# Optimization experiments

Hardware: AMD Instinct MI355X
Metric: run time of the kernel (lower is better)

Reference implementation:

```python
import jax, jax.numpy as jnp
import numpy as np

NUM_HEADS = 16


def setup_inputs() -> dict:
    key = jax.random.key(0)
    ks = jax.random.split(key, 5)
    B, N, D = 2, 2048, 1024
    scale = 1.0 / np.sqrt(D)  # roughly xavier-ish magnitude for weights
    return {
        "x": jax.random.normal(ks[0], (B, N, D), dtype=jnp.float32),
        "W_query": jax.random.normal(ks[1], (D, D), dtype=jnp.float32) * scale,
        "W_key": jax.random.normal(ks[2], (D, D), dtype=jnp.float32) * scale,
        "W_value": jax.random.normal(ks[3], (D, D), dtype=jnp.float32) * scale,
        "W_output": jax.random.normal(ks[4], (D, D), dtype=jnp.float32) * scale,
    }


def reference(x, W_query, W_key, W_value, W_output):
    # x: [B, N, D]; weights: [D, D]
    B, N, D = x.shape
    H = NUM_HEADS
    hd = D // H

    def mh_embed(W):
        # linear_embedding then split heads: [B, N, D] -> [B, H, N, hd]
        y = jnp.einsum("bnd,de->bne", x, W)
        return y.reshape(B, N, H, hd).transpose(0, 2, 1, 3)

    q = mh_embed(W_query)
    k = mh_embed(W_key)
    v = mh_embed(W_value)

    # NOTE: source scales by token_dim**-0.5 (full model dim), not head_dim
    attn = jnp.einsum("bhnd,bhmd->bhnm", q, k) * (D ** -0.5)
    attn = jax.nn.softmax(attn, axis=-1)
    out = jnp.einsum("bhnm,bhmd->bhnd", attn, v)  # [B, H, N, hd]

    out = out.transpose(0, 2, 1, 3).reshape(B, N, D)  # merge heads
    out = jnp.einsum("bnd,de->bne", out, W_output)
    return out
```

## Files before the change

### kernel.cpp

```cpp
#include <hip/hip_runtime.h>

#define D_MODEL 1024
#define N_TOK   2048
#define NHEAD   16
#define HDIM    64
#define BATCH   2
#define M_TOT   (BATCH*N_TOK)

typedef unsigned short u16;
typedef __bf16 bf16x8 __attribute__((ext_vector_type(8)));
typedef float  f32x4  __attribute__((ext_vector_type(4)));

#define QSCALE 0.04508422002777439f

__device__ __forceinline__ u16 f2bf(float f) {
  union { float f; unsigned u; } v; v.f = f;
  unsigned r = v.u + 0x7fffu + ((v.u >> 16) & 1u);
  return (u16)(r >> 16);
}

__device__ __forceinline__ unsigned pk2bf(float a, float b) {
#if __has_builtin(__builtin_amdgcn_cvt_pk_bf16_f32)
  typedef __bf16 bf16x2_t __attribute__((ext_vector_type(2)));
  bf16x2_t r = __builtin_amdgcn_cvt_pk_bf16_f32(a, b);
  union { bf16x2_t v; unsigned u; } c; c.v = r; return c.u;
#else
  return (unsigned)f2bf(a) | ((unsigned)f2bf(b) << 16);
#endif
}

__device__ __forceinline__ void gl2lds16(const void* g, void* l) {
  __builtin_amdgcn_global_load_lds(
      (__attribute__((address_space(1))) void*)g,
      (__attribute__((address_space(3))) void*)l, 16, 0, 0);
}

__global__ void prep_kernel(const float* __restrict__ x,
                            const float* __restrict__ s0, const float* __restrict__ s1,
                            const float* __restrict__ s2, const float* __restrict__ s3,
                            u16* __restrict__ xb,
                            u16* __restrict__ d0, u16* __restrict__ d1,
                            u16* __restrict__ d2, u16* __restrict__ d3) {
  const int t = threadIdx.y * 32 + threadIdx.x;
  if (blockIdx.z == 4) {
    int base = (blockIdx.y * 32 + blockIdx.x) * 256 + t;
#pragma unroll
    for (int r = 0; r < 4; ++r) {
      int i = base + r * 262144;
      float4 v = ((const float4*)x)[i];
      ushort4 o;
      o.x = f2bf(v.x); o.y = f2bf(v.y); o.z = f2bf(v.z); o.w = f2bf(v.w);
      ((ushort4*)xb)[i] = o;
    }
    return;
  }
  const float* src; u16* dst;
  switch (blockIdx.z) {
    case 0:  src = s0; dst = d0; break;
    case 1:  src = s1; dst = d1; break;
    case 2:  src = s2; dst = d2; break;
    default: src = s3; dst = d3; break;
  }
  float sc = (blockIdx.z == 0) ? QSCALE : 1.0f;
  __shared__ float tile[32][33];
  int xg = blockIdx.x * 32 + threadIdx.x;
  int ybase = blockIdx.y * 32;
#pragma unroll
  for (int r = 0; r < 4; ++r)
    tile[threadIdx.y + r*8][threadIdx.x] = src[(size_t)(ybase + threadIdx.y + r*8)*D_MODEL + xg];
  __syncthreads();
#pragma unroll
  for (int r = 0; r < 4; ++r)
    dst[(size_t)(blockIdx.x*32 + threadIdx.y + r*8)*D_MODEL + ybase + threadIdx.x] =
        f2bf(tile[threadIdx.x][threadIdx.y + r*8] * sc);
}

__device__ __forceinline__ void gemm_body(const u16* __restrict__ A,
                                          const u16* __restrict__ Bt,
                                          void* __restrict__ Cout, int mode) {
  __shared__ __attribute__((aligned(16))) u16 lA[128*32];
  __shared__ __attribute__((aligned(16))) u16 lB[128*32];
  const int t = threadIdx.x;
  const int lane = t & 63, w = t >> 6;
  const int wm = w >> 1, wn = w & 1;
  const int q4 = lane >> 4, l15 = lane & 15;
  const int m0 = blockIdx.y * 128, n0 = blockIdx.x * 128;

  f32x4 acc[4][4] = {};

  for (int k0 = 0; k0 < D_MODEL; k0 += 32) {
    __syncthreads();
#pragma unroll
    for (int i = 0; i < 2; ++i) {
      int c = i*256 + t;
      int row = c >> 2;
      int clog = (c & 3) ^ (row & 3);
      gl2lds16(A  + (size_t)(m0 + row)*D_MODEL + k0 + clog*8, lA + c*8);
      gl2lds16(Bt + (size_t)(n0 + row)*D_MODEL + k0 + clog*8, lB + c*8);
    }
    __syncthreads();
    bf16x8 af[4], bfr[4];
#pragma unroll
    for (int mi = 0; mi < 4; ++mi) {
      int r = wm*64 + mi*16 + l15;
      af[mi] = *(const bf16x8*)(lA + r*32 + ((q4 ^ (r & 3)) * 8));
    }
#pragma unroll
    for (int ni = 0; ni < 4; ++ni) {
      int r = wn*64 + ni*16 + l15;
      bfr[ni] = *(const bf16x8*)(lB + r*32 + ((q4 ^ (r & 3)) * 8));
    }
#pragma unroll
    for (int mi = 0; mi < 4; ++mi)
#pragma unroll
      for (int ni = 0; ni < 4; ++ni)
        acc[mi][ni] = __builtin_amdgcn_mfma_f32_16x16x32_bf16(af[mi], bfr[ni], acc[mi][ni], 0, 0, 0);
  }

#pragma unroll
  for (int mi = 0; mi < 4; ++mi) {
#pragma unroll
    for (int ni = 0; ni < 4; ++ni) {
      const int tok0 = m0 + wm*64 + mi*16 + q4*4;
      const int col  = n0 + wn*64 + ni*16 + l15;
      if (mode == 0) {
        u16* D = (u16*)Cout;
#pragma unroll
        for (int r = 0; r < 4; ++r) {
          int tok = tok0 + r;
          int b = tok >> 11, n = tok & (N_TOK-1);
          int h = col >> 6, d = col & (HDIM-1);
          D[(((size_t)(b*NHEAD + h))*N_TOK + n)*HDIM + d] = f2bf(acc[mi][ni][r]);
        }
      } else if (mode == 2) {
        int b = tok0 >> 11, n = tok0 & (N_TOK-1);
        int h = col >> 6, d = col & (HDIM-1);
        ushort4 pk;
        pk.x = f2bf(acc[mi][ni][0]); pk.y = f2bf(acc[mi][ni][1]);
        pk.z = f2bf(acc[mi][ni][2]); pk.w = f2bf(acc[mi][ni][3]);
        *(ushort4*)((u16*)Cout + ((size_t)(b*NHEAD + h)*HDIM + d)*N_TOK + n) = pk;
      } else {
        float* D = (float*)Cout;
#pragma unroll
        for (int r = 0; r < 4; ++r)
          D[(size_t)(tok0 + r)*D_MODEL + col] = acc[mi][ni][r];
      }
    }
  }
}

__global__ __launch_bounds__(256) void qkv_kernel(const u16* __restrict__ xb,
    const u16* __restrict__ wqt, const u16* __restrict__ wkt, const u16* __restrict__ wvt,
    u16* __restrict__ Q, u16* __restrict__ K, u16* __restrict__ Vt) {
  int z = blockIdx.z;
  const u16* B = (z == 0) ? wqt : (z == 1) ? wkt : wvt;
  void* C = (z == 0) ? (void*)Q : (z == 1) ? (void*)K : (void*)Vt;
  gemm_body(xb, B, C, (z == 2) ? 2 : 0);
}

__global__ __launch_bounds__(256) void out_kernel(const u16* __restrict__ ctx,
    const u16* __restrict__ wot, float* __restrict__ out) {
  gemm_body(ctx, wot, (void*)out, 3);
}

__global__ __launch_bounds__(256, 3) void attn_kernel(const u16* __restrict__ Qg,
    const u16* __restrict__ Kg, const u16* __restrict__ Vtg,
    float* __restrict__ Opart, float* __restrict__ Lpart) {
  __shared__ __attribute__((aligned(16))) u16 lds[24576];
  u16* lK = lds;
  u16* lV = lds + 8192;
  u16* lP = lds + 16384;
  const int t = threadIdx.x;
  const int lane = t & 63, w = t >> 6;
  const int q4 = lane >> 4, l15 = lane & 15;
  const int bh = blockIdx.y;
  const int qb = blockIdx.x >> 1, half = blockIdx.x & 1;
  const int qw0 = qb * 128 + w * 32;
  const size_t kvBase = (size_t)bh * (N_TOK * HDIM);
  u16* myP = lP + w * 2048;

  bf16x8 qf[2][2];
#pragma unroll
  for (int ni = 0; ni < 2; ++ni)
#pragma unroll
    for (int kk = 0; kk < 2; ++kk)
      qf[ni][kk] = *(const bf16x8*)(Qg + kvBase +
                    (size_t)(qw0 + ni*16 + l15)*HDIM + kk*32 + q4*8);

  f32x4 accO[4][2] = {};
  float lsum[2] = {0.f, 0.f};

  for (int it = 0; it < 8; ++it) {
    const int kv0 = half * 1024 + it * 128;
    __syncthreads();
#pragma unroll
    for (int i = 0; i < 4; ++i) {
      int c = i*256 + t;
      { int r = c >> 3, ch = c & 7;
        gl2lds16(Kg + kvBase + (size_t)(kv0 + r)*HDIM + ((ch ^ (r & 7)) * 8),
                 lK + c*8); }
      { int d = c >> 4, cv = c & 15;
        gl2lds16(Vtg + kvBase + (size_t)d*N_TOK + kv0 + ((cv ^ (d & 15)) * 8),
                 lV + c*8); }
    }
    __syncthreads();

#pragma unroll
    for (int h = 0; h < 2; ++h) {
#pragma unroll
      for (int mip = 0; mip < 4; ++mip) {
        const int mi = h*4 + mip;
        const int kv = mi*16 + l15;
        f32x4 s[2] = {};
#pragma unroll
        for (int kk = 0; kk < 2; ++kk) {
          bf16x8 a = *(const bf16x8*)(lK + kv*64 + (((kk*4 + q4) ^ (l15 & 7)) * 8));
#pragma unroll
          for (int ni = 0; ni < 2; ++ni)
            s[ni] = __builtin_amdgcn_mfma_f32_16x16x32_bf16(a, qf[ni][kk], s[ni], 0, 0, 0);
        }
#pragma unroll
        for (int ni = 0; ni < 2; ++ni) {
          float p0 = __builtin_amdgcn_exp2f(s[ni][0]);
          float p1 = __builtin_amdgcn_exp2f(s[ni][1]);
          float p2 = __builtin_amdgcn_exp2f(s[ni][2]);
          float p3 = __builtin_amdgcn_exp2f(s[ni][3]);
          lsum[ni] += (p0 + p1) + (p2 + p3);
          uint2 u; u.x = pk2bf(p0, p1); u.y = pk2bf(p2, p3);
          const int qloc = ni*16 + l15;
          const int kv8 = mip*4 + q4;
          *(uint2*)(myP + qloc*64 + (((kv8 >> 1) ^ (qloc & 7)) * 8) + (kv8 & 1)*4) = u;
        }
      }
#pragma unroll
      for (int kk2p = 0; kk2p < 2; ++kk2p) {
        bf16x8 bp[2];
#pragma unroll
        for (int ni = 0; ni < 2; ++ni)
          bp[ni] = *(const bf16x8*)(myP + (ni*16 + l15)*64 +
                                    (((kk2p*4 + q4) ^ (l15 & 7)) * 8));
#pragma unroll
        for (int mi2 = 0; mi2 < 4; ++mi2) {
          const int d = mi2*16 + l15;
          const int g = (h*2 + kk2p)*4 + q4;
          bf16x8 av = *(const bf16x8*)(lV + d*128 + ((g ^ (d & 15)) * 8));
#pragma unroll
          for (int ni = 0; ni < 2; ++ni)
            accO[mi2][ni] = __builtin_amdgcn_mfma_f32_16x16x32_bf16(av, bp[ni], accO[mi2][ni], 0, 0, 0);
        }
      }
    }
  }

  const int b = bh >> 4, head = bh & (NHEAD-1);
  float* Obase = Opart + (size_t)half * (M_TOT * D_MODEL);
#pragma unroll
  for (int ni = 0; ni < 2; ++ni) {
    float ls = lsum[ni];
    ls += __shfl_xor(ls, 16);
    ls += __shfl_xor(ls, 32);
    const int q = qw0 + ni*16 + l15;
    if (q4 == 0)
      Lpart[(size_t)half*(32*N_TOK) + bh*N_TOK + q] = ls;
    const size_t rb = ((size_t)(b*N_TOK + q))*D_MODEL + head*HDIM + q4*4;
#pragma unroll
    for (int mi2 = 0; mi2 < 4; ++mi2) {
      float4 v;
      v.x = accO[mi2][ni][0]; v.y = accO[mi2][ni][1];
      v.z = accO[mi2][ni][2]; v.w = accO[mi2][ni][3];
      *(float4*)(Obase + rb + mi2*16) = v;
    }
  }
}

__global__ __launch_bounds__(256) void combine_kernel(const float* __restrict__ Opart,
    const float* __restrict__ Lpart, u16* __restrict__ ctx) {
  int i = blockIdx.x * 256 + threadIdx.x;
  int tok = i >> 8, d4 = i & 255;
  int n = tok & (N_TOK-1), b = tok >> 11;
  int h = d4 >> 4;
  int bh = b*NHEAD + h;
  float l = Lpart[(size_t)bh*N_TOK + n] + Lpart[(size_t)(32*N_TOK) + bh*N_TOK + n];
  float inv = 1.0f / l;
  float4 o0 = *(const float4*)(Opart + (size_t)tok*D_MODEL + d4*4);
  float4 o1 = *(const float4*)(Opart + (size_t)(M_TOT*D_MODEL) + (size_t)tok*D_MODEL + d4*4);
  ushort4 o;
  o.x = f2bf((o0.x + o1.x) * inv);
  o.y = f2bf((o0.y + o1.y) * inv);
  o.z = f2bf((o0.z + o1.z) * inv);
  o.w = f2bf((o0.w + o1.w) * inv);
  *(ushort4*)(ctx + (size_t)tok*D_MODEL + d4*4) = o;
}

extern "C" void kernel_launch(void* const* d_in, const int* in_sizes, int n_in,
                              void* d_out, int out_size, void* d_ws, size_t ws_size,
                              hipStream_t stream) {
  const float* x  = (const float*)d_in[0];
  const float* Wq = (const float*)d_in[1];
  const float* Wk = (const float*)d_in[2];
  const float* Wv = (const float*)d_in[3];
  const float* Wo = (const float*)d_in[4];
  float* out = (float*)d_out;

  char* ws = (char*)d_ws;
  u16* xb   = (u16*)(ws);
  u16* wqt  = (u16*)(ws + (8u  << 20));
  u16* wkt  = (u16*)(ws + (10u << 20));
  u16* wvt  = (u16*)(ws + (12u << 20));
  u16* wot  = (u16*)(ws + (14u << 20));
  u16* Qw   = (u16*)(ws + (16u << 20));
  u16* Kw   = (u16*)(ws + (24u << 20));
  u16* Vtw  = (u16*)(ws + (32u << 20));
  u16* ctx  = (u16*)(ws + (40u << 20));
  float* Op = (float*)(ws + (48u << 20));
  float* Lp = (float*)(ws + (80u << 20));
  (void)in_sizes; (void)n_in; (void)out_size; (void)ws_size;

  prep_kernel<<<dim3(32, 32, 5), dim3(32, 8), 0, stream>>>(x, Wq, Wk, Wv, Wo,
                                                           xb, wqt, wkt, wvt, wot);
  qkv_kernel<<<dim3(8, 32, 3), 256, 0, stream>>>(xb, wqt, wkt, wvt, Qw, Kw, Vtw);
  attn_kernel<<<dim3(32, 32), 256, 0, stream>>>(Qw, Kw, Vtw, Op, Lp);
  combine_kernel<<<4096, 256, 0, stream>>>(Op, Lp, ctx);
  out_kernel<<<dim3(8, 32), 256, 0, stream>>>(ctx, wot, out);
}
```

Before: 203.1 us.

## Double-buffer LDS tiles in GEMM and attention to overlap loads with MFMA

Both the projection GEMM and the attention kernel now use two LDS buffers. The global-to-LDS loads for the next K step (GEMM) or KV tile (attention) are issued before the MFMA work on the current buffer, which removes one barrier per iteration and hides load latency. To keep total LDS the same, the attention KV tile shrinks from 128 to 64 tokens, with twice the iterations and a narrower V swizzle. The trade-off is more loop iterations and barriers in attention, plus doubled LDS in the GEMM, which may lower occupancy.

```diff
diff --git a/kernel.cpp b/kernel.cpp
--- a/kernel.cpp
+++ b/kernel.cpp
@@ -78,37 +78,47 @@
 __device__ __forceinline__ void gemm_body(const u16* __restrict__ A,
                                           const u16* __restrict__ Bt,
                                           void* __restrict__ Cout, int mode) {
-  __shared__ __attribute__((aligned(16))) u16 lA[128*32];
-  __shared__ __attribute__((aligned(16))) u16 lB[128*32];
+  __shared__ __attribute__((aligned(16))) u16 lA[2][128*32];
+  __shared__ __attribute__((aligned(16))) u16 lB[2][128*32];
   const int t = threadIdx.x;
   const int lane = t & 63, w = t >> 6;
   const int wm = w >> 1, wn = w & 1;
   const int q4 = lane >> 4, l15 = lane & 15;
   const int m0 = blockIdx.y * 128, n0 = blockIdx.x * 128;
 
+  const int c0 = t, c1 = 256 + t;
+  const int r0 = c0 >> 2, g0 = (c0 & 3) ^ (r0 & 3);
+  const int r1 = c1 >> 2, g1 = (c1 & 3) ^ (r1 & 3);
+
   f32x4 acc[4][4] = {};
 
-  for (int k0 = 0; k0 < D_MODEL; k0 += 32) {
+  gl2lds16(A  + (size_t)(m0 + r0)*D_MODEL + g0*8, &lA[0][c0*8]);
+  gl2lds16(Bt + (size_t)(n0 + r0)*D_MODEL + g0*8, &lB[0][c0*8]);
+  gl2lds16(A  + (size_t)(m0 + r1)*D_MODEL + g1*8, &lA[0][c1*8]);
+  gl2lds16(Bt + (size_t)(n0 + r1)*D_MODEL + g1*8, &lB[0][c1*8]);
+
+  for (int it = 0; it < 32; ++it) {
+    const int cur = it & 1;
     __syncthreads();
-#pragma unroll
-    for (int i = 0; i < 2; ++i) {
-      int c = i*256 + t;
-      int row = c >> 2;
-      int clog = (c & 3) ^ (row & 3);
-      gl2lds16(A  + (size_t)(m0 + row)*D_MODEL + k0 + clog*8, lA + c*8);
-      gl2lds16(Bt + (size_t)(n0 + row)*D_MODEL + k0 + clog*8, lB + c*8);
-    }
-    __syncthreads();
+    if (it + 1 < 32) {
+      const int kn = (it + 1) * 32;
+      u16* dA = &lA[cur ^ 1][0]; u16* dB = &lB[cur ^ 1][0];
+      gl2lds16(A  + (size_t)(m0 + r0)*D_MODEL + kn + g0*8, dA + c0*8);
+      gl2lds16(Bt + (size_t)(n0 + r0)*D_MODEL + kn + g0*8, dB + c0*8);
+      gl2lds16(A  + (size_t)(m0 + r1)*D_MODEL + kn + g1*8, dA + c1*8);
+      gl2lds16(Bt + (size_t)(n0 + r1)*D_MODEL + kn + g1*8, dB + c1*8);
+    }
+    const u16* sA = &lA[cur][0]; const u16* sB = &lB[cur][0];
     bf16x8 af[4], bfr[4];
 #pragma unroll
     for (int mi = 0; mi < 4; ++mi) {
       int r = wm*64 + mi*16 + l15;
-      af[mi] = *(const bf16x8*)(lA + r*32 + ((q4 ^ (r & 3)) * 8));
+      af[mi] = *(const bf16x8*)(sA + r*32 + ((q4 ^ (r & 3)) * 8));
     }
 #pragma unroll
     for (int ni = 0; ni < 4; ++ni) {
       int r = wn*64 + ni*16 + l15;
-      bfr[ni] = *(const bf16x8*)(lB + r*32 + ((q4 ^ (r & 3)) * 8));
+      bfr[ni] = *(const bf16x8*)(sB + r*32 + ((q4 ^ (r & 3)) * 8));
     }
 #pragma unroll
     for (int mi = 0; mi < 4; ++mi)
@@ -167,9 +177,6 @@
     const u16* __restrict__ Kg, const u16* __restrict__ Vtg,
     float* __restrict__ Opart, float* __restrict__ Lpart) {
   __shared__ __attribute__((aligned(16))) u16 lds[24576];
-  u16* lK = lds;
-  u16* lV = lds + 8192;
-  u16* lP = lds + 16384;
   const int t = threadIdx.x;
   const int lane = t & 63, w = t >> 6;
   const int q4 = lane >> 4, l15 = lane & 15;
@@ -177,7 +184,11 @@
   const int qb = blockIdx.x >> 1, half = blockIdx.x & 1;
   const int qw0 = qb * 128 + w * 32;
   const size_t kvBase = (size_t)bh * (N_TOK * HDIM);
-  u16* myP = lP + w * 2048;
+  u16* myP = lds + 16384 + w * 2048;
+
+  const int ck0 = t, ck1 = 256 + t;
+  const int kr0 = ck0 >> 3, kg0 = (ck0 & 7) ^ (kr0 & 7);
+  const int kr1 = ck1 >> 3, kg1 = (ck1 & 7) ^ (kr1 & 7);
 
   bf16x8 qf[2][2];
 #pragma unroll
@@ -190,64 +201,66 @@
   f32x4 accO[4][2] = {};
   float lsum[2] = {0.f, 0.f};
 
-  for (int it = 0; it < 8; ++it) {
-    const int kv0 = half * 1024 + it * 128;
+  const int kvStart = half * 1024;
+  gl2lds16(Kg  + kvBase + (size_t)(kvStart + kr0)*HDIM + kg0*8, lds + ck0*8);
+  gl2lds16(Kg  + kvBase + (size_t)(kvStart + kr1)*HDIM + kg1*8, lds + ck1*8);
+  gl2lds16(Vtg + kvBase + (size_t)kr0*N_TOK + kvStart + kg0*8,  lds + 8192 + ck0*8);
+  gl2lds16(Vtg + kvBase + (size_t)kr1*N_TOK + kvStart + kg1*8,  lds + 8192 + ck1*8);
+
+  for (int it = 0; it < 16; ++it) {
+    const int cur = it & 1;
     __syncthreads();
-#pragma unroll
-    for (int i = 0; i < 4; ++i) {
-      int c = i*256 + t;
-      { int r = c >> 3, ch = c & 7;
-        gl2lds16(Kg + kvBase + (size_t)(kv0 + r)*HDIM + ((ch ^ (r & 7)) * 8),
-                 lK + c*8); }
-      { int d = c >> 4, cv = c & 15;
-        gl2lds16(Vtg + kvBase + (size_t)d*N_TOK + kv0 + ((cv ^ (d & 15)) * 8),
-                 lV + c*8); }
-    }
-    __syncthreads();
-
-#pragma unroll
-    for (int h = 0; h < 2; ++h) {
-#pragma unroll
-      for (int mip = 0; mip < 4; ++mip) {
-        const int mi = h*4 + mip;
-        const int kv = mi*16 + l15;
-        f32x4 s[2] = {};
-#pragma unroll
-        for (int kk = 0; kk < 2; ++kk) {
-          bf16x8 a = *(const bf16x8*)(lK + kv*64 + (((kk*4 + q4) ^ (l15 & 7)) * 8));
-#pragma unroll
-          for (int ni = 0; ni < 2; ++ni)
-            s[ni] = __builtin_amdgcn_mfma_f32_16x16x32_bf16(a, qf[ni][kk], s[ni], 0, 0, 0);
-        }
-#pragma unroll
-        for (int ni = 0; ni < 2; ++ni) {
-          float p0 = __builtin_amdgcn_exp2f(s[ni][0]);
-          float p1 = __builtin_amdgcn_exp2f(s[ni][1]);
-          float p2 = __builtin_amdgcn_exp2f(s[ni][2]);
-          float p3 = __builtin_amdgcn_exp2f(s[ni][3]);
-          lsum[ni] += (p0 + p1) + (p2 + p3);
-          uint2 u; u.x = pk2bf(p0, p1); u.y = pk2bf(p2, p3);
-          const int qloc = ni*16 + l15;
-          const int kv8 = mip*4 + q4;
-          *(uint2*)(myP + qloc*64 + (((kv8 >> 1) ^ (qloc & 7)) * 8) + (kv8 & 1)*4) = u;
-        }
+    if (it + 1 < 16) {
+      const int kvn = kvStart + (it + 1) * 64;
+      u16* dK = lds + (cur ^ 1) * 4096;
+      u16* dV = lds + 8192 + (cur ^ 1) * 4096;
+      gl2lds16(Kg  + kvBase + (size_t)(kvn + kr0)*HDIM + kg0*8, dK + ck0*8);
+      gl2lds16(Kg  + kvBase + (size_t)(kvn + kr1)*HDIM + kg1*8, dK + ck1*8);
+      gl2lds16(Vtg + kvBase + (size_t)kr0*N_TOK + kvn + kg0*8,  dV + ck0*8);
+      gl2lds16(Vtg + kvBase + (size_t)kr1*N_TOK + kvn + kg1*8,  dV + ck1*8);
+    }
+    const u16* sK = lds + cur * 4096;
+    const u16* sV = lds + 8192 + cur * 4096;
+
+#pragma unroll
+    for (int mip = 0; mip < 4; ++mip) {
+      const int kv = mip*16 + l15;
+      f32x4 s[2] = {};
+#pragma unroll
+      for (int kk = 0; kk < 2; ++kk) {
+        bf16x8 a = *(const bf16x8*)(sK + kv*64 + (((kk*4 + q4) ^ (l15 & 7)) * 8));
+#pragma unroll
+        for (int ni = 0; ni < 2; ++ni)
+          s[ni] = __builtin_amdgcn_mfma_f32_16x16x32_bf16(a, qf[ni][kk], s[ni], 0, 0, 0);
       }
 #pragma unroll
-      for (int kk2p = 0; kk2p < 2; ++kk2p) {
-        bf16x8 bp[2];
+      for (int ni = 0; ni < 2; ++ni) {
+        float p0 = __builtin_amdgcn_exp2f(s[ni][0]);
+        float p1 = __builtin_amdgcn_exp2f(s[ni][1]);
+        float p2 = __builtin_amdgcn_exp2f(s[ni][2]);
+        float p3 = __builtin_amdgcn_exp2f(s[ni][3]);
+        lsum[ni] += (p0 + p1) + (p2 + p3);
+        uint2 u; u.x = pk2bf(p0, p1); u.y = pk2bf(p2, p3);
+        const int qloc = ni*16 + l15;
+        const int kv8 = mip*4 + q4;
+        *(uint2*)(myP + qloc*64 + (((kv8 >> 1) ^ (qloc & 7)) * 8) + (kv8 & 1)*4) = u;
+      }
+    }
+
+#pragma unroll
+    for (int kk2 = 0; kk2 < 2; ++kk2) {
+      bf16x8 bp[2];
+#pragma unroll
+      for (int ni = 0; ni < 2; ++ni)
+        bp[ni] = *(const bf16x8*)(myP + (ni*16 + l15)*64 +
+                                  (((kk2*4 + q4) ^ (l15 & 7)) * 8));
+#pragma unroll
+      for (int mi2 = 0; mi2 < 4; ++mi2) {
+        const int d = mi2*16 + l15;
+        bf16x8 av = *(const bf16x8*)(sV + d*64 + (((kk2*4 + q4) ^ (d & 7)) * 8));
 #pragma unroll
         for (int ni = 0; ni < 2; ++ni)
-          bp[ni] = *(const bf16x8*)(myP + (ni*16 + l15)*64 +
-                                    (((kk2p*4 + q4) ^ (l15 & 7)) * 8));
-#pragma unroll
-        for (int mi2 = 0; mi2 < 4; ++mi2) {
-          const int d = mi2*16 + l15;
-          const int g = (h*2 + kk2p)*4 + q4;
-          bf16x8 av = *(const bf16x8*)(lV + d*128 + ((g ^ (d & 15)) * 8));
-#pragma unroll
-          for (int ni = 0; ni < 2; ++ni)
-            accO[mi2][ni] = __builtin_amdgcn_mfma_f32_16x16x32_bf16(av, bp[ni], accO[mi2][ni], 0, 0, 0);
-        }
+          accO[mi2][ni] = __builtin_amdgcn_mfma_f32_16x16x32_bf16(av, bp[ni], accO[mi2][ni], 0, 0, 0);
       }
     }
   }
```

After: 204.5 us. Within noise of the previous version (+0.7%).
